# Performance work log

Hardware: AMD Instinct MI355X
Metric: run time of the kernel (lower is better)

The kernel has to match this reference:

```python
import jax, jax.numpy as jnp
import numpy as np

E, D_IN, D_OUT, N = 8, 1024, 1024, 8192

def setup_inputs() -> dict:
    key = jax.random.key(0)
    ks = jax.random.split(key, 5)
    s_in = 1.0 / np.sqrt(D_IN)
    x = jax.random.normal(ks[0], (N, D_IN), dtype=jnp.float32)
    We = jax.random.uniform(ks[1], (E, D_IN, D_OUT), dtype=jnp.float32, minval=-s_in, maxval=s_in)
    be = jax.random.uniform(ks[2], (E, D_OUT), dtype=jnp.float32, minval=-s_in, maxval=s_in)
    Wg = jax.random.uniform(ks[3], (D_IN, E), dtype=jnp.float32, minval=-s_in, maxval=s_in)
    bg = jax.random.uniform(ks[4], (E,), dtype=jnp.float32, minval=-s_in, maxval=s_in)
    return {"x": x, "We": We, "be": be, "Wg": Wg, "bg": bg}

def reference(x, We, be, Wg, bg):
    # experts_outputs: [N, E, D_OUT] (stacked per-expert Linear outputs)
    expert_out = jnp.einsum('ni,eio->neo', x, We) + be[None, :, :]
    # gate: softmax over experts, [N, E]
    gate = jax.nn.softmax(x @ Wg + bg, axis=1)
    # weighted combine (bmm of [N,1,E] x [N,E,D_OUT]) -> [N, D_OUT]
    return jnp.einsum('ne,neo->no', gate, expert_out)
```

## Files before the change

kernel.cpp:

```cpp
#include <hip/hip_runtime.h>
#include <hip/hip_bf16.h>
#include <cstdint>

#define NTOK 8192
#define DIN  1024
#define DOUT 1024
#define NEXP 8

typedef __attribute__((ext_vector_type(8))) __bf16 bf16x8;
typedef __attribute__((ext_vector_type(4))) float f32x4;

__device__ __forceinline__ unsigned short f2bf(float f) {
    unsigned int u = __builtin_bit_cast(unsigned int, f);
    u += 0x7FFFu + ((u >> 16) & 1u);
    return (unsigned short)(u >> 16);
}

__device__ __forceinline__ void cp16(const void* gsrc, void* ldst) {
    __builtin_amdgcn_global_load_lds(
        (const __attribute__((address_space(1))) void*)gsrc,
        (__attribute__((address_space(3))) void*)ldst,
        16, 0, 0);
}

__global__ __launch_bounds__(256) void gate_convx_kernel(
    const float* __restrict__ x, const float* __restrict__ Wg,
    const float* __restrict__ bg, unsigned short* __restrict__ xb,
    float* __restrict__ g)
{
    int lane = threadIdx.x & 63;
    int wave = threadIdx.x >> 6;
    int n = blockIdx.x * 4 + wave;

    const float* xr = x + (size_t)n * DIN;
    unsigned short* xbr = xb + (size_t)n * DIN;

    float a0=0,a1=0,a2=0,a3=0,a4=0,a5=0,a6=0,a7=0;

#pragma unroll
    for (int c = 0; c < 4; ++c) {
        int k = c * 256 + lane * 4;
        float4 v = *(const float4*)&xr[k];
        ushort4 u;
        u.x = f2bf(v.x); u.y = f2bf(v.y); u.z = f2bf(v.z); u.w = f2bf(v.w);
        *(ushort4*)&xbr[k] = u;
#pragma unroll
        for (int i = 0; i < 4; ++i) {
            float xv = (i == 0) ? v.x : (i == 1) ? v.y : (i == 2) ? v.z : v.w;
            float4 w0 = *(const float4*)&Wg[(size_t)(k + i) * NEXP];
            float4 w1 = *(const float4*)&Wg[(size_t)(k + i) * NEXP + 4];
            a0 += xv * w0.x; a1 += xv * w0.y; a2 += xv * w0.z; a3 += xv * w0.w;
            a4 += xv * w1.x; a5 += xv * w1.y; a6 += xv * w1.z; a7 += xv * w1.w;
        }
    }

#pragma unroll
    for (int off = 32; off > 0; off >>= 1) {
        a0 += __shfl_xor(a0, off, 64);
        a1 += __shfl_xor(a1, off, 64);
        a2 += __shfl_xor(a2, off, 64);
        a3 += __shfl_xor(a3, off, 64);
        a4 += __shfl_xor(a4, off, 64);
        a5 += __shfl_xor(a5, off, 64);
        a6 += __shfl_xor(a6, off, 64);
        a7 += __shfl_xor(a7, off, 64);
    }

    float l[8] = {a0,a1,a2,a3,a4,a5,a6,a7};
    float m = -1e30f;
#pragma unroll
    for (int e = 0; e < 8; ++e) { l[e] += bg[e]; m = fmaxf(m, l[e]); }
    float s = 0.f;
#pragma unroll
    for (int e = 0; e < 8; ++e) { l[e] = __expf(l[e] - m); s += l[e]; }
    float inv = 1.0f / s;

    if (lane == 0) {
        float4 p0 = make_float4(l[0]*inv, l[1]*inv, l[2]*inv, l[3]*inv);
        float4 p1 = make_float4(l[4]*inv, l[5]*inv, l[6]*inv, l[7]*inv);
        *(float4*)&g[(size_t)n * 8]     = p0;
        *(float4*)&g[(size_t)n * 8 + 4] = p1;
    }
}

__global__ __launch_bounds__(256) void conv_we_kernel(
    const float* __restrict__ We, unsigned short* __restrict__ wt)
{
    __shared__ unsigned short tile[64 * 72];

    int b = blockIdx.x;
    int e  = b >> 8;
    int kt = (b >> 4) & 15;
    int ot = b & 15;

    const float* src = We + ((size_t)e << 20) + (size_t)(kt * 64) * DOUT + ot * 64;
    unsigned short* dst = wt + ((size_t)e << 20) + (size_t)(ot * 64) * DIN + kt * 64;

    int t = threadIdx.x;
    int kl = t >> 2;
    int og = (t & 3) * 16;
#pragma unroll
    for (int c = 0; c < 4; ++c) {
        int o = og + c * 4;
        float4 v = *(const float4*)&src[(size_t)kl * DOUT + o];
        ushort4 u;
        u.x = f2bf(v.x); u.y = f2bf(v.y); u.z = f2bf(v.z); u.w = f2bf(v.w);
        *(ushort4*)&tile[kl * 72 + o] = u;
    }
    __syncthreads();
    int ol = t >> 2;
    int kg = (t & 3) * 16;
    unsigned short tmp[16];
#pragma unroll
    for (int i = 0; i < 16; ++i) tmp[i] = tile[(kg + i) * 72 + ol];
    *(uint4*)&dst[(size_t)ol * DIN + kg]     = *(uint4*)&tmp[0];
    *(uint4*)&dst[(size_t)ol * DIN + kg + 8] = *(uint4*)&tmp[8];
}

__global__ __launch_bounds__(256, 2) void moe_gemm_kernel(
    const unsigned short* __restrict__ xb,
    const unsigned short* __restrict__ wt,
    const float* __restrict__ g,
    const float* __restrict__ be,
    float* __restrict__ out)
{
    __shared__ unsigned short lA[128 * 64];
    __shared__ unsigned short lB[128 * 64];
    __shared__ float lG[128 * 8];
    __shared__ float lBias[8 * 128];

    int bid = blockIdx.x;
    int bm = (bid & 7) * 8 + ((bid >> 3) & 7);
    int bn = bid >> 6;
    int tid = threadIdx.x;
    int lane = tid & 63;
    int wave = tid >> 6;
    int wm = wave >> 1;
    int wn = wave & 1;

    {
        *(float4*)&lG[tid * 4] = *(const float4*)&g[(size_t)(bm * 128) * 8 + tid * 4];
#pragma unroll
        for (int q = 0; q < 4; ++q) {
            int idx = q * 256 + tid;
            lBias[idx] = be[(size_t)(idx >> 7) * DOUT + bn * 128 + (idx & 127)];
        }
    }

    f32x4 outAcc[4][4] = {};

    const unsigned short* aBase = xb + (size_t)(bm * 128) * DIN;
    const unsigned short* bBase0 = wt + (size_t)(bn * 128) * DIN;

    int rowS = wave * 8 + (lane >> 3);
    int k8   = (((lane & 7) ^ (lane >> 3)) * 8);
    int rA   = lane & 15;
    int swz  = rA & 7;

    for (int e = 0; e < NEXP; ++e) {
        f32x4 acc[4][4] = {};
        const unsigned short* bBase = bBase0 + ((size_t)e << 20);

        for (int kt = 0; kt < 16; ++kt) {
            int kb = kt * 64;
            __syncthreads();
#pragma unroll
            for (int j = 0; j < 4; ++j) {
                int row = j * 32 + rowS;
                cp16(aBase + (size_t)row * DIN + kb + k8,
                     &lA[j * 2048 + wave * 512]);
                cp16(bBase + (size_t)row * DIN + kb + k8,
                     &lB[j * 2048 + wave * 512]);
            }
            __syncthreads();
#pragma unroll
            for (int ks = 0; ks < 2; ++ks) {
                int kc = ks * 4 + (lane >> 4);
                int kp = (kc ^ swz) * 8;
                bf16x8 af[4], bfr[4];
#pragma unroll
                for (int i = 0; i < 4; ++i)
                    af[i] = *(const bf16x8*)&lA[(wm * 64 + i * 16 + rA) * 64 + kp];
#pragma unroll
                for (int j = 0; j < 4; ++j)
                    bfr[j] = *(const bf16x8*)&lB[(wn * 64 + j * 16 + rA) * 64 + kp];
#pragma unroll
                for (int i = 0; i < 4; ++i)
#pragma unroll
                    for (int j = 0; j < 4; ++j)
                        acc[i][j] = __builtin_amdgcn_mfma_f32_16x16x32_bf16(
                            af[i], bfr[j], acc[i][j], 0, 0, 0);
            }
        }

        float bv[4];
#pragma unroll
        for (int j = 0; j < 4; ++j)
            bv[j] = lBias[e * 128 + wn * 64 + j * 16 + rA];
#pragma unroll
        for (int i = 0; i < 4; ++i) {
            int rb = wm * 64 + i * 16 + (lane >> 4) * 4;
            float g0 = lG[(rb + 0) * 8 + e];
            float g1 = lG[(rb + 1) * 8 + e];
            float g2 = lG[(rb + 2) * 8 + e];
            float g3 = lG[(rb + 3) * 8 + e];
#pragma unroll
            for (int j = 0; j < 4; ++j) {
                outAcc[i][j].x += g0 * (acc[i][j].x + bv[j]);
                outAcc[i][j].y += g1 * (acc[i][j].y + bv[j]);
                outAcc[i][j].z += g2 * (acc[i][j].z + bv[j]);
                outAcc[i][j].w += g3 * (acc[i][j].w + bv[j]);
            }
        }
    }

#pragma unroll
    for (int i = 0; i < 4; ++i) {
        int rowb = bm * 128 + wm * 64 + i * 16 + (lane >> 4) * 4;
#pragma unroll
        for (int j = 0; j < 4; ++j) {
            int col = bn * 128 + wn * 64 + j * 16 + rA;
            out[(size_t)(rowb + 0) * DOUT + col] = outAcc[i][j].x;
            out[(size_t)(rowb + 1) * DOUT + col] = outAcc[i][j].y;
            out[(size_t)(rowb + 2) * DOUT + col] = outAcc[i][j].z;
            out[(size_t)(rowb + 3) * DOUT + col] = outAcc[i][j].w;
        }
    }
}

extern "C" void kernel_launch(void* const* d_in, const int* in_sizes, int n_in,
                              void* d_out, int out_size, void* d_ws, size_t ws_size,
                              hipStream_t stream)
{
    const float* x  = (const float*)d_in[0];
    const float* We = (const float*)d_in[1];
    const float* be = (const float*)d_in[2];
    const float* Wg = (const float*)d_in[3];
    const float* bg = (const float*)d_in[4];
    float* out = (float*)d_out;

    unsigned short* xb = (unsigned short*)d_ws;
    unsigned short* wt = xb + (size_t)NTOK * DIN;
    float* g = (float*)(wt + (size_t)NEXP * DOUT * DIN);

    gate_convx_kernel<<<NTOK / 4, 256, 0, stream>>>(x, Wg, bg, xb, g);
    conv_we_kernel<<<NEXP * 16 * 16, 256, 0, stream>>>(We, wt);
    moe_gemm_kernel<<<(NTOK / 128) * (DOUT / 128), 256, 0, stream>>>(xb, wt, g, be, out);
}
```

Measured before the change: 264.2 us.

## Merge prep kernels and switch GEMM to 32x32x16 MFMA with 128-wide K tiles

The two preprocessing kernels become one launch: the first 2048 blocks transpose and convert We to bf16, and the remaining blocks convert x to bf16 and compute the softmax gate from tiles staged in LDS. The main GEMM moves from 16x16x32 to 32x32x16 bf16 MFMA, doubles the K tile to 128 with a new XOR swizzle, and halves the number of barrier pairs. Gate weights and bias are now read straight from global memory instead of LDS. The aim is fewer launches, fewer LDS fragment loads per MFMA and less synchronisation, at the cost of twice the LDS per block, which may lower occupancy.

```diff
diff --git a/kernel.cpp b/kernel.cpp
--- a/kernel.cpp
+++ b/kernel.cpp
@@ -7,8 +7,9 @@
 #define DOUT 1024
 #define NEXP 8
 
-typedef __attribute__((ext_vector_type(8))) __bf16 bf16x8;
-typedef __attribute__((ext_vector_type(4))) float f32x4;
+typedef __attribute__((ext_vector_type(8)))  __bf16 bf16x8;
+typedef __attribute__((ext_vector_type(4)))  float  f32x4;
+typedef __attribute__((ext_vector_type(16))) float  f32x16;
 
 __device__ __forceinline__ unsigned short f2bf(float f) {
     unsigned int u = __builtin_bit_cast(unsigned int, f);
@@ -23,98 +24,108 @@
         16, 0, 0);
 }
 
-__global__ __launch_bounds__(256) void gate_convx_kernel(
-    const float* __restrict__ x, const float* __restrict__ Wg,
-    const float* __restrict__ bg, unsigned short* __restrict__ xb,
+__global__ __launch_bounds__(256) void prep_kernel(
+    const float* __restrict__ x, const float* __restrict__ We,
+    const float* __restrict__ Wg, const float* __restrict__ bg,
+    unsigned short* __restrict__ xb, unsigned short* __restrict__ wt,
     float* __restrict__ g)
 {
-    int lane = threadIdx.x & 63;
-    int wave = threadIdx.x >> 6;
-    int n = blockIdx.x * 4 + wave;
-
-    const float* xr = x + (size_t)n * DIN;
-    unsigned short* xbr = xb + (size_t)n * DIN;
-
-    float a0=0,a1=0,a2=0,a3=0,a4=0,a5=0,a6=0,a7=0;
-
-#pragma unroll
-    for (int c = 0; c < 4; ++c) {
-        int k = c * 256 + lane * 4;
-        float4 v = *(const float4*)&xr[k];
-        ushort4 u;
-        u.x = f2bf(v.x); u.y = f2bf(v.y); u.z = f2bf(v.z); u.w = f2bf(v.w);
-        *(ushort4*)&xbr[k] = u;
-#pragma unroll
-        for (int i = 0; i < 4; ++i) {
-            float xv = (i == 0) ? v.x : (i == 1) ? v.y : (i == 2) ? v.z : v.w;
-            float4 w0 = *(const float4*)&Wg[(size_t)(k + i) * NEXP];
-            float4 w1 = *(const float4*)&Wg[(size_t)(k + i) * NEXP + 4];
-            a0 += xv * w0.x; a1 += xv * w0.y; a2 += xv * w0.z; a3 += xv * w0.w;
-            a4 += xv * w1.x; a5 += xv * w1.y; a6 += xv * w1.z; a7 += xv * w1.w;
+    __shared__ float smem[12416];
+
+    int t = threadIdx.x;
+
+    if (blockIdx.x < 2048) {
+        unsigned short* tile = (unsigned short*)smem;
+        int b = blockIdx.x;
+        int e  = b >> 8;
+        int kt = (b >> 4) & 15;
+        int ot = b & 15;
+
+        const float* src = We + ((size_t)e << 20) + (size_t)(kt * 64) * DOUT + ot * 64;
+        unsigned short* dst = wt + ((size_t)e << 20) + (size_t)(ot * 64) * DIN + kt * 64;
+
+        int kl = t >> 2;
+        int og = (t & 3) * 16;
+#pragma unroll
+        for (int c = 0; c < 4; ++c) {
+            int o = og + c * 4;
+            float4 v = *(const float4*)&src[(size_t)kl * DOUT + o];
+            ushort4 u;
+            u.x = f2bf(v.x); u.y = f2bf(v.y); u.z = f2bf(v.z); u.w = f2bf(v.w);
+            *(ushort4*)&tile[kl * 72 + o] = u;
+        }
+        __syncthreads();
+        int ol = t >> 2;
+        int kg = (t & 3) * 16;
+        unsigned short tmp[16];
+#pragma unroll
+        for (int i = 0; i < 16; ++i) tmp[i] = tile[(kg + i) * 72 + ol];
+        *(uint4*)&dst[(size_t)ol * DIN + kg]     = *(uint4*)&tmp[0];
+        *(uint4*)&dst[(size_t)ol * DIN + kg + 8] = *(uint4*)&tmp[8];
+    } else {
+        float* WgL = smem;
+        float* xL  = smem + 8192;
+        int n0 = (blockIdx.x - 2048) * 32;
+
+#pragma unroll
+        for (int q = 0; q < 8; ++q) {
+            int fidx = q * 256 + t;
+            int k  = fidx >> 1;
+            int eh = (fidx & 1) * 4;
+            float4 v = *(const float4*)&Wg[(size_t)k * 8 + eh];
+            WgL[(eh + 0) * 1024 + k] = v.x;
+            WgL[(eh + 1) * 1024 + k] = v.y;
+            WgL[(eh + 2) * 1024 + k] = v.z;
+            WgL[(eh + 3) * 1024 + k] = v.w;
+        }
+
+        int tt = t & 31;
+        int e  = t >> 5;
+        float acc = 0.f;
+
+        for (int c = 0; c < 8; ++c) {
+            int kb = c * 128;
+#pragma unroll
+            for (int q = 0; q < 4; ++q) {
+                int fidx = q * 256 + t;
+                int row = fidx >> 5;
+                int kk  = (fidx & 31) * 4;
+                float4 v = *(const float4*)&x[(size_t)(n0 + row) * DIN + kb + kk];
+                ushort4 u;
+                u.x = f2bf(v.x); u.y = f2bf(v.y); u.z = f2bf(v.z); u.w = f2bf(v.w);
+                *(ushort4*)&xb[(size_t)(n0 + row) * DIN + kb + kk] = u;
+                *(float4*)&xL[row * 132 + kk] = v;
+            }
+            __syncthreads();
+#pragma unroll
+            for (int kk = 0; kk < 128; kk += 4) {
+                float4 xv = *(const float4*)&xL[tt * 132 + kk];
+                float4 wv = *(const float4*)&WgL[e * 1024 + kb + kk];
+                acc += xv.x * wv.x + xv.y * wv.y + xv.z * wv.z + xv.w * wv.w;
+            }
+            __syncthreads();
+        }
+
+        float* lg = xL;
+        lg[tt * 8 + e] = acc + bg[e];
+        __syncthreads();
+        if (t < 32) {
+            float l[8];
+#pragma unroll
+            for (int i = 0; i < 8; ++i) l[i] = lg[t * 8 + i];
+            float m = l[0];
+#pragma unroll
+            for (int i = 1; i < 8; ++i) m = fmaxf(m, l[i]);
+            float s = 0.f;
+#pragma unroll
+            for (int i = 0; i < 8; ++i) { l[i] = __expf(l[i] - m); s += l[i]; }
+            float inv = 1.0f / s;
+            float4 p0 = make_float4(l[0]*inv, l[1]*inv, l[2]*inv, l[3]*inv);
+            float4 p1 = make_float4(l[4]*inv, l[5]*inv, l[6]*inv, l[7]*inv);
+            *(float4*)&g[(size_t)(n0 + t) * 8]     = p0;
+            *(float4*)&g[(size_t)(n0 + t) * 8 + 4] = p1;
         }
     }
-
-#pragma unroll
-    for (int off = 32; off > 0; off >>= 1) {
-        a0 += __shfl_xor(a0, off, 64);
-        a1 += __shfl_xor(a1, off, 64);
-        a2 += __shfl_xor(a2, off, 64);
-        a3 += __shfl_xor(a3, off, 64);
-        a4 += __shfl_xor(a4, off, 64);
-        a5 += __shfl_xor(a5, off, 64);
-        a6 += __shfl_xor(a6, off, 64);
-        a7 += __shfl_xor(a7, off, 64);
-    }
-
-    float l[8] = {a0,a1,a2,a3,a4,a5,a6,a7};
-    float m = -1e30f;
-#pragma unroll
-    for (int e = 0; e < 8; ++e) { l[e] += bg[e]; m = fmaxf(m, l[e]); }
-    float s = 0.f;
-#pragma unroll
-    for (int e = 0; e < 8; ++e) { l[e] = __expf(l[e] - m); s += l[e]; }
-    float inv = 1.0f / s;
-
-    if (lane == 0) {
-        float4 p0 = make_float4(l[0]*inv, l[1]*inv, l[2]*inv, l[3]*inv);
-        float4 p1 = make_float4(l[4]*inv, l[5]*inv, l[6]*inv, l[7]*inv);
-        *(float4*)&g[(size_t)n * 8]     = p0;
-        *(float4*)&g[(size_t)n * 8 + 4] = p1;
-    }
-}
-
-__global__ __launch_bounds__(256) void conv_we_kernel(
-    const float* __restrict__ We, unsigned short* __restrict__ wt)
-{
-    __shared__ unsigned short tile[64 * 72];
-
-    int b = blockIdx.x;
-    int e  = b >> 8;
-    int kt = (b >> 4) & 15;
-    int ot = b & 15;
-
-    const float* src = We + ((size_t)e << 20) + (size_t)(kt * 64) * DOUT + ot * 64;
-    unsigned short* dst = wt + ((size_t)e << 20) + (size_t)(ot * 64) * DIN + kt * 64;
-
-    int t = threadIdx.x;
-    int kl = t >> 2;
-    int og = (t & 3) * 16;
-#pragma unroll
-    for (int c = 0; c < 4; ++c) {
-        int o = og + c * 4;
-        float4 v = *(const float4*)&src[(size_t)kl * DOUT + o];
-        ushort4 u;
-        u.x = f2bf(v.x); u.y = f2bf(v.y); u.z = f2bf(v.z); u.w = f2bf(v.w);
-        *(ushort4*)&tile[kl * 72 + o] = u;
-    }
-    __syncthreads();
-    int ol = t >> 2;
-    int kg = (t & 3) * 16;
-    unsigned short tmp[16];
-#pragma unroll
-    for (int i = 0; i < 16; ++i) tmp[i] = tile[(kg + i) * 72 + ol];
-    *(uint4*)&dst[(size_t)ol * DIN + kg]     = *(uint4*)&tmp[0];
-    *(uint4*)&dst[(size_t)ol * DIN + kg + 8] = *(uint4*)&tmp[8];
 }
 
 __global__ __launch_bounds__(256, 2) void moe_gemm_kernel(
@@ -124,10 +135,8 @@
     const float* __restrict__ be,
     float* __restrict__ out)
 {
-    __shared__ unsigned short lA[128 * 64];
-    __shared__ unsigned short lB[128 * 64];
-    __shared__ float lG[128 * 8];
-    __shared__ float lBias[8 * 128];
+    __shared__ unsigned short lA[128 * 128];
+    __shared__ unsigned short lB[128 * 128];
 
     int bid = blockIdx.x;
     int bm = (bid & 7) * 8 + ((bid >> 3) & 7);
@@ -138,94 +147,96 @@
     int wm = wave >> 1;
     int wn = wave & 1;
 
-    {
-        *(float4*)&lG[tid * 4] = *(const float4*)&g[(size_t)(bm * 128) * 8 + tid * 4];
-#pragma unroll
-        for (int q = 0; q < 4; ++q) {
-            int idx = q * 256 + tid;
-            lBias[idx] = be[(size_t)(idx >> 7) * DOUT + bn * 128 + (idx & 127)];
-        }
-    }
-
-    f32x4 outAcc[4][4] = {};
-
     const unsigned short* aBase = xb + (size_t)(bm * 128) * DIN;
     const unsigned short* bBase0 = wt + (size_t)(bn * 128) * DIN;
 
-    int rowS = wave * 8 + (lane >> 3);
-    int k8   = (((lane & 7) ^ (lane >> 3)) * 8);
-    int rA   = lane & 15;
-    int swz  = rA & 7;
-
+    int lrow  = lane >> 4;
+    int cphys = lane & 15;
+    int row7  = (((wave & 1) * 4) + lrow) & 7;
+    int clog  = cphys ^ row7;
+
+    int col  = lane & 31;
+    int half = lane >> 5;
+
+    f32x16 outAcc[2][2] = {};
+
+#pragma unroll 1
     for (int e = 0; e < NEXP; ++e) {
-        f32x4 acc[4][4] = {};
+        f32x16 acc[2][2] = {};
         const unsigned short* bBase = bBase0 + ((size_t)e << 20);
 
-        for (int kt = 0; kt < 16; ++kt) {
-            int kb = kt * 64;
-            __syncthreads();
-#pragma unroll
-            for (int j = 0; j < 4; ++j) {
-                int row = j * 32 + rowS;
-                cp16(aBase + (size_t)row * DIN + kb + k8,
-                     &lA[j * 2048 + wave * 512]);
-                cp16(bBase + (size_t)row * DIN + kb + k8,
-                     &lB[j * 2048 + wave * 512]);
-            }
-            __syncthreads();
-#pragma unroll
-            for (int ks = 0; ks < 2; ++ks) {
-                int kc = ks * 4 + (lane >> 4);
-                int kp = (kc ^ swz) * 8;
-                bf16x8 af[4], bfr[4];
-#pragma unroll
-                for (int i = 0; i < 4; ++i)
-                    af[i] = *(const bf16x8*)&lA[(wm * 64 + i * 16 + rA) * 64 + kp];
-#pragma unroll
-                for (int j = 0; j < 4; ++j)
-                    bfr[j] = *(const bf16x8*)&lB[(wn * 64 + j * 16 + rA) * 64 + kp];
-#pragma unroll
-                for (int i = 0; i < 4; ++i)
-#pragma unroll
-                    for (int j = 0; j < 4; ++j)
-                        acc[i][j] = __builtin_amdgcn_mfma_f32_16x16x32_bf16(
+#pragma unroll 1
+        for (int kt = 0; kt < 8; ++kt) {
+            int kb = kt * 128;
+            __syncthreads();
+#pragma unroll
+            for (int s = 0; s < 8; ++s) {
+                int R0 = s * 16 + wave * 4;
+                size_t srcOff = (size_t)(R0 + lrow) * DIN + kb + clog * 8;
+                cp16(aBase + srcOff, &lA[R0 * 128]);
+                cp16(bBase + srcOff, &lB[R0 * 128]);
+            }
+            __syncthreads();
+#pragma unroll
+            for (int ks = 0; ks < 8; ++ks) {
+                int cl = ks * 2 + half;
+                bf16x8 af[2], bfr[2];
+#pragma unroll
+                for (int i = 0; i < 2; ++i) {
+                    int m = wm * 64 + i * 32 + col;
+                    af[i] = *(const bf16x8*)&lA[m * 128 + (cl ^ (m & 7)) * 8];
+                }
+#pragma unroll
+                for (int j = 0; j < 2; ++j) {
+                    int o = wn * 64 + j * 32 + col;
+                    bfr[j] = *(const bf16x8*)&lB[o * 128 + (cl ^ (o & 7)) * 8];
+                }
+#pragma unroll
+                for (int i = 0; i < 2; ++i)
+#pragma unroll
+                    for (int j = 0; j < 2; ++j)
+                        acc[i][j] = __builtin_amdgcn_mfma_f32_32x32x16_bf16(
                             af[i], bfr[j], acc[i][j], 0, 0, 0);
             }
         }
 
-        float bv[4];
-#pragma unroll
-        for (int j = 0; j < 4; ++j)
-            bv[j] = lBias[e * 128 + wn * 64 + j * 16 + rA];
-#pragma unroll
-        for (int i = 0; i < 4; ++i) {
-            int rb = wm * 64 + i * 16 + (lane >> 4) * 4;
-            float g0 = lG[(rb + 0) * 8 + e];
-            float g1 = lG[(rb + 1) * 8 + e];
-            float g2 = lG[(rb + 2) * 8 + e];
-            float g3 = lG[(rb + 3) * 8 + e];
-#pragma unroll
-            for (int j = 0; j < 4; ++j) {
-                outAcc[i][j].x += g0 * (acc[i][j].x + bv[j]);
-                outAcc[i][j].y += g1 * (acc[i][j].y + bv[j]);
-                outAcc[i][j].z += g2 * (acc[i][j].z + bv[j]);
-                outAcc[i][j].w += g3 * (acc[i][j].w + bv[j]);
+        float bv[2];
+#pragma unroll
+        for (int j = 0; j < 2; ++j)
+            bv[j] = be[(size_t)e * DOUT + bn * 128 + wn * 64 + j * 32 + col];
+#pragma unroll
+        for (int i = 0; i < 2; ++i) {
+#pragma unroll
+            for (int q = 0; q < 4; ++q) {
+                int rbase = bm * 128 + wm * 64 + i * 32 + q * 8 + half * 4;
+                float g0 = g[(size_t)(rbase + 0) * 8 + e];
+                float g1 = g[(size_t)(rbase + 1) * 8 + e];
+                float g2 = g[(size_t)(rbase + 2) * 8 + e];
+                float g3 = g[(size_t)(rbase + 3) * 8 + e];
+#pragma unroll
+                for (int j = 0; j < 2; ++j) {
+                    outAcc[i][j][q * 4 + 0] += g0 * (acc[i][j][q * 4 + 0] + bv[j]);
+                    outAcc[i][j][q * 4 + 1] += g1 * (acc[i][j][q * 4 + 1] + bv[j]);
+                    outAcc[i][j][q * 4 + 2] += g2 * (acc[i][j][q * 4 + 2] + bv[j]);
+                    outAcc[i][j][q * 4 + 3] += g3 * (acc[i][j][q * 4 + 3] + bv[j]);
+                }
             }
         }
     }
 
 #pragma unroll
-    for (int i = 0; i < 4; ++i) {
-        int rowb = bm * 128 + wm * 64 + i * 16 + (lane >> 4) * 4;
-#pragma unroll
-        for (int j = 0; j < 4; ++j) {
-            int col = bn * 128 + wn * 64 + j * 16 + rA;
-            out[(size_t)(rowb + 0) * DOUT + col] = outAcc[i][j].x;
-            out[(size_t)(rowb + 1) * DOUT + col] = outAcc[i][j].y;
-            out[(size_t)(rowb + 2) * DOUT + col] = outAcc[i][j].z;
-            out[(size_t)(rowb + 3) * DOUT + col] = outAcc[i][j].w;
-        }
-    }
+    for (int i = 0; i < 2; ++i)
+#pragma unroll
+        for (int q = 0; q < 4; ++q) {
+            int row = bm * 128 + wm * 64 + i * 32 + q * 8 + half * 4;
+#pragma unroll
+            for (int j = 0; j < 2; ++j) {
+                int c = bn * 128 + wn * 64 + j * 32 + col;
+#pragma unroll
+                for (int r = 0; r < 4; ++r)
+                    out[(size_t)(row + r) * DOUT + c] = outAcc[i][j][q * 4 + r];
+            }
+        }
 }
 
 extern "C" void kernel_launch(void* const* d_in, const int* in_sizes, int n_in,
@@ -243,7 +254,6 @@
     unsigned short* wt = xb + (size_t)NTOK * DIN;
     float* g = (float*)(wt + (size_t)NEXP * DOUT * DIN);
 
-    gate_convx_kernel<<<NTOK / 4, 256, 0, stream>>>(x, Wg, bg, xb, g);
-    conv_we_kernel<<<NEXP * 16 * 16, 256, 0, stream>>>(We, wt);
+    prep_kernel<<<2048 + 256, 256, 0, stream>>>(x, We, Wg, bg, xb, wt, g);
     moe_gemm_kernel<<<(NTOK / 128) * (DOUT / 128), 256, 0, stream>>>(xb, wt, g, be, out);
 }
```

Result: slower. 283.6 us (+7.3%).
